# Kernel optimization log

Hardware: AMD Instinct MI355X
Metric: run time of the kernel (lower is better)

## Reference

```python
import jax, jax.numpy as jnp
import numpy as np

B = 256       # number of grasp centers (batch)
N = 65536     # total points output by the backbone
C = 1024      # backbone feature channels (enc_channels[-1])
K = 512       # padded slots per segment (points per center)
INFO = 3      # info_size
KCLS = 6      # k_cls
EPS = 1e-5    # LayerNorm eps


def _layernorm(x, g, b):
    m = x.mean(-1, keepdims=True)
    v = ((x - m) ** 2).mean(-1, keepdims=True)
    return (x - m) / jnp.sqrt(v + EPS) * g + b


def setup_inputs() -> dict:
    key = jax.random.key(0)
    ks = jax.random.split(key, 10)
    feat = jax.random.normal(ks[0], (N, C), jnp.float32)
    offsets = jnp.sort(jax.random.randint(ks[1], (B,), 0, N)).astype(jnp.int64)
    offsets = offsets.at[-1].set(N)  # cumulative ends, last covers all points
    info = jax.random.normal(ks[2], (B, INFO), jnp.float32)

    def lin(k, o, i):
        return 0.02 * jax.random.normal(k, (o, i), jnp.float32), jnp.zeros((o,), jnp.float32)

    W1, b1 = lin(ks[3], 512, C)          # point_layer Linear(1024,512)
    Wi, bi = lin(ks[4], 32, INFO)        # info_layer Linear(info_size,32)
    Wa1, ba1 = lin(ks[5], 256, 544)      # anchor_mlp Linear(544,256)
    Wa2, ba2 = lin(ks[6], KCLS, 256)     # anchor_mlp Linear(256,k_cls)
    Wo1, bo1 = lin(ks[7], 256, 544)      # offset_mlp Linear(544,256)
    Wo2, bo2 = lin(ks[8], KCLS * 3, 256) # offset_mlp Linear(256,k_cls*3)
    return dict(
        feat=feat, info=info, offsets=offsets,
        W1=W1, b1=b1, ln1_g=jnp.ones((512,)), ln1_b=jnp.zeros((512,)),
        Wi=Wi, bi=bi,
        Wa1=Wa1, ba1=ba1, lna_g=jnp.ones((256,)), lna_b=jnp.zeros((256,)),
        Wa2=Wa2, ba2=ba2,
        Wo1=Wo1, bo1=bo1, lno_g=jnp.ones((256,)), lno_b=jnp.zeros((256,)),
        Wo2=Wo2, bo2=bo2,
    )


def reference(feat, info, W1, b1, ln1_g, ln1_b, Wi, bi,
              Wa1, ba1, lna_g, lna_b, Wa2, ba2,
              Wo1, bo1, lno_g, lno_b, Wo2, bo2, offsets):
    # --- fused segment-max replaces the pad loop + max over padded dim ---
    # point i belongs to segment b s.t. offsets[b-1] <= i < offsets[b]
    ids = jnp.searchsorted(offsets, jnp.arange(feat.shape[0]), side='right')
    segmax = jax.ops.segment_max(feat, ids, num_segments=B)  # (B, C)
    lengths = jnp.diff(offsets, prepend=0)
    # original zero-pads to K slots: segments shorter than K see 0 in the max
    features = jnp.where((lengths < K)[:, None], jnp.maximum(segmax, 0.0), segmax)

    # point_layer: Linear -> LayerNorm -> Dropout(eval: identity) -> ReLU
    pf = jax.nn.relu(_layernorm(features @ W1.T + b1, ln1_g, ln1_b))
    # info_layer
    inf = info @ Wi.T + bi
    x = jnp.concatenate([pf, inf], axis=1)  # (B, 544)

    pred = jax.nn.relu(_layernorm(x @ Wa1.T + ba1, lna_g, lna_b)) @ Wa2.T + ba2
    off = jax.nn.relu(_layernorm(x @ Wo1.T + bo1, lno_g, lno_b)) @ Wo2.T + bo2
    offset = off.reshape(-1, KCLS, 3)
    return features, pred, offset
```

## Files before the change

### kernel.cpp

```cpp
#include <hip/hip_runtime.h>
#include <hip/hip_bf16.h>
#include <cstdint>

#define NPTS 65536
#define CCH  1024
#define BSEG 256
#define KSLOT 512

__device__ __forceinline__ int fkey(float f) {
  int i = __float_as_int(f);
  return i >= 0 ? i : (i ^ 0x7FFFFFFF);
}
__device__ __forceinline__ float fdec(int k) {
  int i = k >= 0 ? k : (k ^ 0x7FFFFFFF);
  return __int_as_float(i);
}
#define NEGKEY ((int)0x807FFFFF)

__device__ __forceinline__ float4 max4(float4 a, float4 b) {
  return make_float4(fmaxf(a.x, b.x), fmaxf(a.y, b.y), fmaxf(a.z, b.z), fmaxf(a.w, b.w));
}

__global__ __launch_bounds__(256) void init_keys_k(int* __restrict__ keys) {
  keys[blockIdx.x * 256 + threadIdx.x] = NEGKEY;
}

__global__ __launch_bounds__(256) void segmax_k(const float* __restrict__ feat,
                                                const int* __restrict__ offsets,
                                                int* __restrict__ keys) {
  int t = threadIdx.x;
  int col = t << 2;
  int row0 = blockIdx.x * 64;
  int row_end = row0 + 64;
  int lo = 0, hi = BSEG - 1;
  while (lo < hi) { int mid = (lo + hi) >> 1; if (offsets[mid] > row0) hi = mid; else lo = mid + 1; }
  int seg = lo;
  int end = offsets[seg];
  const float NI = __int_as_float(0xFF800000);
  float4 m = make_float4(NI, NI, NI, NI);
  bool dirty = false;
  int r = row0;
  while (r < row_end) {
    while (r >= end) {
      if (dirty) {
        int* kp = keys + seg * CCH + col;
        atomicMax(kp + 0, fkey(m.x));
        atomicMax(kp + 1, fkey(m.y));
        atomicMax(kp + 2, fkey(m.z));
        atomicMax(kp + 3, fkey(m.w));
        m = make_float4(NI, NI, NI, NI);
        dirty = false;
      }
      ++seg;
      end = offsets[seg];
    }
    int stop = min(row_end, end);
    const float* p = feat + (size_t)r * CCH + col;
    for (; r + 4 <= stop; r += 4) {
      float4 v0 = *(const float4*)(p);
      float4 v1 = *(const float4*)(p + CCH);
      float4 v2 = *(const float4*)(p + 2 * CCH);
      float4 v3 = *(const float4*)(p + 3 * CCH);
      p += 4 * CCH;
      m = max4(m, max4(max4(v0, v1), max4(v2, v3)));
    }
    for (; r < stop; ++r) {
      float4 v = *(const float4*)(p);
      p += CCH;
      m = max4(m, v);
    }
    dirty = true;
  }
  if (dirty) {
    int* kp = keys + seg * CCH + col;
    atomicMax(kp + 0, fkey(m.x));
    atomicMax(kp + 1, fkey(m.y));
    atomicMax(kp + 2, fkey(m.z));
    atomicMax(kp + 3, fkey(m.w));
  }
}

__global__ __launch_bounds__(256) void finalize_k(const int* __restrict__ keys,
                                                  const int* __restrict__ offsets,
                                                  float* __restrict__ outf) {
  int idx = blockIdx.x * 256 + threadIdx.x;
  int b = idx >> 10;
  int len = offsets[b] - (b ? offsets[b - 1] : 0);
  float f = fdec(keys[idx]);
  if (len < KSLOT) f = fmaxf(f, 0.0f);
  outf[idx] = f;
}

__global__ __launch_bounds__(256) void gemm_nt_part(
    const float* __restrict__ A, int lda,
    const float* __restrict__ Wlo, const float* __restrict__ Whi, int nlo, int ldw,
    float* __restrict__ part, int Ktot, int steps_per_chunk) {
  __shared__ float As[32][68];
  __shared__ float Ws[32][68];
  int bx = blockIdx.x, by = blockIdx.y, bz = blockIdx.z;
  int t = threadIdx.x;
  int tx = t & 15, ty = t >> 4;
  int steps_total = Ktot >> 5;
  int step0 = bz * steps_per_chunk;
  int nsteps = min(steps_per_chunk, steps_total - step0);
  int lr = t >> 3;
  int lk = (t & 7) << 2;
  const float* Arow0 = A + (size_t)(by * 64 + lr) * lda + lk;
  const float* Arow1 = Arow0 + (size_t)32 * lda;
  int c0 = bx * 64 + lr;
  int c1 = c0 + 32;
  const float* Wrow0 = (c0 < nlo ? Wlo + (size_t)c0 * ldw : Whi + (size_t)(c0 - nlo) * ldw) + lk;
  const float* Wrow1 = (c1 < nlo ? Wlo + (size_t)c1 * ldw : Whi + (size_t)(c1 - nlo) * ldw) + lk;
  float acc[4][4] = {};
  for (int s = 0; s < nsteps; ++s) {
    int k0 = (step0 + s) << 5;
    float4 a0 = *(const float4*)(Arow0 + k0);
    float4 a1 = *(const float4*)(Arow1 + k0);
    float4 w0 = *(const float4*)(Wrow0 + k0);
    float4 w1 = *(const float4*)(Wrow1 + k0);
    __syncthreads();
    As[lk + 0][lr] = a0.x; As[lk + 1][lr] = a0.y; As[lk + 2][lr] = a0.z; As[lk + 3][lr] = a0.w;
    As[lk + 0][lr + 32] = a1.x; As[lk + 1][lr + 32] = a1.y; As[lk + 2][lr + 32] = a1.z; As[lk + 3][lr + 32] = a1.w;
    Ws[lk + 0][lr] = w0.x; Ws[lk + 1][lr] = w0.y; Ws[lk + 2][lr] = w0.z; Ws[lk + 3][lr] = w0.w;
    Ws[lk + 0][lr + 32] = w1.x; Ws[lk + 1][lr + 32] = w1.y; Ws[lk + 2][lr + 32] = w1.z; Ws[lk + 3][lr + 32] = w1.w;
    __syncthreads();
#pragma unroll
    for (int kk = 0; kk < 32; ++kk) {
      float4 av = *(const float4*)&As[kk][ty << 2];
      float4 wv = *(const float4*)&Ws[kk][tx << 2];
      acc[0][0] += av.x * wv.x; acc[0][1] += av.x * wv.y; acc[0][2] += av.x * wv.z; acc[0][3] += av.x * wv.w;
      acc[1][0] += av.y * wv.x; acc[1][1] += av.y * wv.y; acc[1][2] += av.y * wv.z; acc[1][3] += av.y * wv.w;
      acc[2][0] += av.z * wv.x; acc[2][1] += av.z * wv.y; acc[2][2] += av.z * wv.z; acc[2][3] += av.z * wv.w;
      acc[3][0] += av.w * wv.x; acc[3][1] += av.w * wv.y; acc[3][2] += av.w * wv.z; acc[3][3] += av.w * wv.w;
    }
  }
  float* op = part + (size_t)bz * 131072 + (size_t)(by * 64 + (ty << 2)) * 512 + bx * 64 + (tx << 2);
#pragma unroll
  for (int i = 0; i < 4; ++i) {
    *(float4*)(op + (size_t)i * 512) = make_float4(acc[i][0], acc[i][1], acc[i][2], acc[i][3]);
  }
}

__global__ __launch_bounds__(256) void ln1_x_k(
    const float* __restrict__ part1, const float* __restrict__ b1,
    const float* __restrict__ g, const float* __restrict__ be,
    const float* __restrict__ info, const float* __restrict__ Wi, const float* __restrict__ bi,
    float* __restrict__ x) {
  int b = blockIdx.x, t = threadIdx.x;
  int wv = t >> 6, ln = t & 63;
  __shared__ float red[2][4];
  __shared__ float stats[2];
  const float* p = part1 + (size_t)b * 512;
  float z0 = b1[t] + p[t] + p[131072 + t] + p[262144 + t] + p[393216 + t];
  int c1 = t + 256;
  float z1 = b1[c1] + p[c1] + p[131072 + c1] + p[262144 + c1] + p[393216 + c1];
  float s = z0 + z1, q = z0 * z0 + z1 * z1;
#pragma unroll
  for (int o = 32; o; o >>= 1) { s += __shfl_down(s, o); q += __shfl_down(q, o); }
  if (ln == 0) { red[0][wv] = s; red[1][wv] = q; }
  __syncthreads();
  if (t == 0) {
    float S = red[0][0] + red[0][1] + red[0][2] + red[0][3];
    float Q = red[1][0] + red[1][1] + red[1][2] + red[1][3];
    float mean = S * (1.f / 512.f);
    float var = Q * (1.f / 512.f) - mean * mean;
    stats[0] = mean; stats[1] = rsqrtf(var + 1e-5f);
  }
  __syncthreads();
  float mean = stats[0], rstd = stats[1];
  x[b * 544 + t]  = fmaxf((z0 - mean) * rstd * g[t]  + be[t],  0.f);
  x[b * 544 + c1] = fmaxf((z1 - mean) * rstd * g[c1] + be[c1], 0.f);
  if (t < 32) {
    float i0 = info[b * 3], i1 = info[b * 3 + 1], i2 = info[b * 3 + 2];
    x[b * 544 + 512 + t] = bi[t] + Wi[t * 3] * i0 + Wi[t * 3 + 1] * i1 + Wi[t * 3 + 2] * i2;
  }
}

__global__ __launch_bounds__(256) void heads_k(
    const float* __restrict__ part2,
    const float* __restrict__ ba1, const float* __restrict__ ga, const float* __restrict__ bea,
    const float* __restrict__ Wa2, const float* __restrict__ ba2,
    const float* __restrict__ bo1, const float* __restrict__ go, const float* __restrict__ beo,
    const float* __restrict__ Wo2, const float* __restrict__ bo2,
    float* __restrict__ outp) {
  int b = blockIdx.x, t = threadIdx.x;
  int wv = t >> 6, ln = t & 63;
  __shared__ float h[512];
  __shared__ float red[4][4];
  __shared__ float stats[4];
  const float* p0 = part2 + (size_t)b * 512;
  const float* p1 = p0 + 131072;
  float za = ba1[t] + p0[t] + p1[t];
  float zo = bo1[t] + p0[256 + t] + p1[256 + t];
  float sa = za, qa = za * za, so = zo, qo = zo * zo;
#pragma unroll
  for (int o = 32; o; o >>= 1) {
    sa += __shfl_down(sa, o); qa += __shfl_down(qa, o);
    so += __shfl_down(so, o); qo += __shfl_down(qo, o);
  }
  if (ln == 0) { red[wv][0] = sa; red[wv][1] = qa; red[wv][2] = so; red[wv][3] = qo; }
  __syncthreads();
  if (t == 0) {
    float Sa = red[0][0] + red[1][0] + red[2][0] + red[3][0];
    float Qa = red[0][1] + red[1][1] + red[2][1] + red[3][1];
    float So = red[0][2] + red[1][2] + red[2][2] + red[3][2];
    float Qo = red[0][3] + red[1][3] + red[2][3] + red[3][3];
    float ma = Sa * (1.f / 256.f), va = Qa * (1.f / 256.f) - ma * ma;
    float mo = So * (1.f / 256.f), vo = Qo * (1.f / 256.f) - mo * mo;
    stats[0] = ma; stats[1] = rsqrtf(va + 1e-5f);
    stats[2] = mo; stats[3] = rsqrtf(vo + 1e-5f);
  }
  __syncthreads();
  h[t]       = fmaxf((za - stats[0]) * stats[1] * ga[t] + bea[t], 0.f);
  h[256 + t] = fmaxf((zo - stats[2]) * stats[3] * go[t] + beo[t], 0.f);
  __syncthreads();
  const float* hh = (wv == 0) ? h : (h + 256);
  const float* W2 = (wv == 0) ? Wa2 : Wo2;
  const float* b2 = (wv == 0) ? ba2 : bo2;
  int o0 = (wv == 0) ? 0 : (wv - 1) * 6;
  int base = (wv == 0) ? (262144 + b * 6) : (263680 + b * 18);
  float h0 = hh[ln], h1 = hh[64 + ln], h2v = hh[128 + ln], h3 = hh[192 + ln];
#pragma unroll
  for (int oo = 0; oo < 6; ++oo) {
    int o = o0 + oo;
    const float* w = W2 + o * 256;
    float pr = h0 * w[ln] + h1 * w[64 + ln] + h2v * w[128 + ln] + h3 * w[192 + ln];
#pragma unroll
    for (int d = 32; d; d >>= 1) pr += __shfl_down(pr, d);
    if (ln == 0) outp[base + o] = pr + b2[o];
  }
}

extern "C" void kernel_launch(void* const* d_in, const int* in_sizes, int n_in,
                              void* d_out, int out_size, void* d_ws, size_t ws_size,
                              hipStream_t stream) {
  const float* feat   = (const float*)d_in[0];
  const float* info   = (const float*)d_in[1];
  const int*   offs   = (const int*)d_in[2];
  const float* W1     = (const float*)d_in[3];
  const float* b1     = (const float*)d_in[4];
  const float* ln1_g  = (const float*)d_in[5];
  const float* ln1_b  = (const float*)d_in[6];
  const float* Wi     = (const float*)d_in[7];
  const float* bi     = (const float*)d_in[8];
  const float* Wa1    = (const float*)d_in[9];
  const float* ba1    = (const float*)d_in[10];
  const float* lna_g  = (const float*)d_in[11];
  const float* lna_b  = (const float*)d_in[12];
  const float* Wa2    = (const float*)d_in[13];
  const float* ba2    = (const float*)d_in[14];
  const float* Wo1    = (const float*)d_in[15];
  const float* bo1    = (const float*)d_in[16];
  const float* lno_g  = (const float*)d_in[17];
  const float* lno_b  = (const float*)d_in[18];
  const float* Wo2    = (const float*)d_in[19];
  const float* bo2    = (const float*)d_in[20];

  char* ws = (char*)d_ws;
  int*   keys  = (int*)ws;
  float* part1 = (float*)(ws + (1u << 20));
  float* xbuf  = (float*)(ws + 3u * (1u << 20));
  float* part2 = (float*)(ws + 3u * (1u << 20) + 655360u);
  float* features = (float*)d_out;
  float* outp = (float*)d_out;

  init_keys_k<<<dim3(1024), dim3(256), 0, stream>>>(keys);
  segmax_k<<<dim3(1024), dim3(256), 0, stream>>>(feat, offs, keys);
  finalize_k<<<dim3(1024), dim3(256), 0, stream>>>(keys, offs, features);
  gemm_nt_part<<<dim3(8, 4, 4), dim3(256), 0, stream>>>(
      features, 1024, W1, W1, 512, 1024, part1, 1024, 8);
  ln1_x_k<<<dim3(256), dim3(256), 0, stream>>>(part1, b1, ln1_g, ln1_b, info, Wi, bi, xbuf);
  gemm_nt_part<<<dim3(8, 4, 2), dim3(256), 0, stream>>>(
      xbuf, 544, Wa1, Wo1, 256, 544, part2, 544, 9);
  heads_k<<<dim3(256), dim3(256), 0, stream>>>(
      part2, ba1, lna_g, lna_b, Wa2, ba2, bo1, lno_g, lno_b, Wo2, bo2, outp);
}
```

Before: 99.91 us.

## Fuse segmax finalize into first GEMM, use memset and nontemporal loads

Removes the finalize kernel by decoding the unsigned order-preserving max keys and applying the zero-pad clamp inside the first GEMM's A-tile load. Blocks with bx==0 also write the features output. The key encoding changes to unsigned so a plain hipMemsetAsync of zero can replace the init kernel. The segment-max kernel now covers 32 rows per block with twice as many blocks, unrolls its loop 8 rows deep, and reads feat with nontemporal loads. This cuts two launches and one pass over the key buffer, at the cost of more atomics and redundant decode work in every GEMM block.

```diff
diff --git a/kernel.cpp b/kernel.cpp
--- a/kernel.cpp
+++ b/kernel.cpp
@@ -6,49 +6,57 @@
 #define CCH  1024
 #define BSEG 256
 #define KSLOT 512
-
-__device__ __forceinline__ int fkey(float f) {
+#define WROWS 32
+
+typedef float v4f __attribute__((ext_vector_type(4)));
+
+__device__ __forceinline__ unsigned ukey(float f) {
   int i = __float_as_int(f);
-  return i >= 0 ? i : (i ^ 0x7FFFFFFF);
-}
-__device__ __forceinline__ float fdec(int k) {
-  int i = k >= 0 ? k : (k ^ 0x7FFFFFFF);
-  return __int_as_float(i);
-}
-#define NEGKEY ((int)0x807FFFFF)
-
-__device__ __forceinline__ float4 max4(float4 a, float4 b) {
-  return make_float4(fmaxf(a.x, b.x), fmaxf(a.y, b.y), fmaxf(a.z, b.z), fmaxf(a.w, b.w));
-}
-
-__global__ __launch_bounds__(256) void init_keys_k(int* __restrict__ keys) {
-  keys[blockIdx.x * 256 + threadIdx.x] = NEGKEY;
+  return i >= 0 ? ((unsigned)i | 0x80000000u) : ~(unsigned)i;
+}
+__device__ __forceinline__ float udec(unsigned u, bool rl) {
+  float v;
+  if (u >= 0x80000000u) v = __int_as_float((int)(u & 0x7FFFFFFFu));
+  else                  v = __int_as_float((int)~u);
+  if (u == 0u) v = -__builtin_inff();
+  if (rl) v = fmaxf(v, 0.0f);
+  return v;
+}
+
+__device__ __forceinline__ v4f ntload4(const float* p) {
+  return __builtin_nontemporal_load((const v4f*)p);
+}
+__device__ __forceinline__ v4f vmax4(v4f a, v4f b) {
+  v4f r;
+  r.x = fmaxf(a.x, b.x); r.y = fmaxf(a.y, b.y);
+  r.z = fmaxf(a.z, b.z); r.w = fmaxf(a.w, b.w);
+  return r;
 }
 
 __global__ __launch_bounds__(256) void segmax_k(const float* __restrict__ feat,
                                                 const int* __restrict__ offsets,
-                                                int* __restrict__ keys) {
+                                                unsigned* __restrict__ keys) {
   int t = threadIdx.x;
   int col = t << 2;
-  int row0 = blockIdx.x * 64;
-  int row_end = row0 + 64;
+  int row0 = blockIdx.x * WROWS;
+  int row_end = row0 + WROWS;
   int lo = 0, hi = BSEG - 1;
   while (lo < hi) { int mid = (lo + hi) >> 1; if (offsets[mid] > row0) hi = mid; else lo = mid + 1; }
   int seg = lo;
   int end = offsets[seg];
-  const float NI = __int_as_float(0xFF800000);
-  float4 m = make_float4(NI, NI, NI, NI);
+  const float NI = -__builtin_inff();
+  v4f m; m.x = NI; m.y = NI; m.z = NI; m.w = NI;
   bool dirty = false;
   int r = row0;
   while (r < row_end) {
     while (r >= end) {
       if (dirty) {
-        int* kp = keys + seg * CCH + col;
-        atomicMax(kp + 0, fkey(m.x));
-        atomicMax(kp + 1, fkey(m.y));
-        atomicMax(kp + 2, fkey(m.z));
-        atomicMax(kp + 3, fkey(m.w));
-        m = make_float4(NI, NI, NI, NI);
+        unsigned* kp = keys + (size_t)seg * CCH + col;
+        atomicMax(kp + 0, ukey(m.x));
+        atomicMax(kp + 1, ukey(m.y));
+        atomicMax(kp + 2, ukey(m.z));
+        atomicMax(kp + 3, ukey(m.w));
+        m.x = NI; m.y = NI; m.z = NI; m.w = NI;
         dirty = false;
       }
       ++seg;
@@ -56,39 +64,89 @@
     }
     int stop = min(row_end, end);
     const float* p = feat + (size_t)r * CCH + col;
-    for (; r + 4 <= stop; r += 4) {
-      float4 v0 = *(const float4*)(p);
-      float4 v1 = *(const float4*)(p + CCH);
-      float4 v2 = *(const float4*)(p + 2 * CCH);
-      float4 v3 = *(const float4*)(p + 3 * CCH);
-      p += 4 * CCH;
-      m = max4(m, max4(max4(v0, v1), max4(v2, v3)));
+    for (; r + 8 <= stop; r += 8) {
+      v4f v0 = ntload4(p);
+      v4f v1 = ntload4(p + CCH);
+      v4f v2 = ntload4(p + 2 * CCH);
+      v4f v3 = ntload4(p + 3 * CCH);
+      v4f v4 = ntload4(p + 4 * CCH);
+      v4f v5 = ntload4(p + 5 * CCH);
+      v4f v6 = ntload4(p + 6 * CCH);
+      v4f v7 = ntload4(p + 7 * CCH);
+      p += 8 * CCH;
+      m = vmax4(m, vmax4(vmax4(vmax4(v0, v1), vmax4(v2, v3)),
+                         vmax4(vmax4(v4, v5), vmax4(v6, v7))));
     }
     for (; r < stop; ++r) {
-      float4 v = *(const float4*)(p);
+      v4f v = ntload4(p);
       p += CCH;
-      m = max4(m, v);
+      m = vmax4(m, v);
     }
     dirty = true;
   }
   if (dirty) {
-    int* kp = keys + seg * CCH + col;
-    atomicMax(kp + 0, fkey(m.x));
-    atomicMax(kp + 1, fkey(m.y));
-    atomicMax(kp + 2, fkey(m.z));
-    atomicMax(kp + 3, fkey(m.w));
-  }
-}
-
-__global__ __launch_bounds__(256) void finalize_k(const int* __restrict__ keys,
-                                                  const int* __restrict__ offsets,
-                                                  float* __restrict__ outf) {
-  int idx = blockIdx.x * 256 + threadIdx.x;
-  int b = idx >> 10;
-  int len = offsets[b] - (b ? offsets[b - 1] : 0);
-  float f = fdec(keys[idx]);
-  if (len < KSLOT) f = fmaxf(f, 0.0f);
-  outf[idx] = f;
+    unsigned* kp = keys + (size_t)seg * CCH + col;
+    atomicMax(kp + 0, ukey(m.x));
+    atomicMax(kp + 1, ukey(m.y));
+    atomicMax(kp + 2, ukey(m.z));
+    atomicMax(kp + 3, ukey(m.w));
+  }
+}
+
+__global__ __launch_bounds__(256) void gemm1_fused(
+    const unsigned* __restrict__ keys, const int* __restrict__ offsets,
+    const float* __restrict__ W1, float* __restrict__ features,
+    float* __restrict__ part) {
+  __shared__ float As[32][68];
+  __shared__ float Ws[32][68];
+  int bx = blockIdx.x, by = blockIdx.y, bz = blockIdx.z;
+  int t = threadIdx.x;
+  int tx = t & 15, ty = t >> 4;
+  int lr = t >> 3;
+  int lk = (t & 7) << 2;
+  int row0 = by * 64 + lr, row1 = row0 + 32;
+  int len0 = offsets[row0] - (row0 ? offsets[row0 - 1] : 0);
+  int len1 = offsets[row1] - offsets[row1 - 1];
+  bool rl0 = len0 < KSLOT, rl1 = len1 < KSLOT;
+  const unsigned* K0 = keys + (size_t)row0 * CCH + lk;
+  const unsigned* K1 = keys + (size_t)row1 * CCH + lk;
+  int c0 = bx * 64 + lr, c1 = c0 + 32;
+  const float* Wr0 = W1 + (size_t)c0 * CCH + lk;
+  const float* Wr1 = W1 + (size_t)c1 * CCH + lk;
+  float acc[4][4] = {};
+  for (int s = 0; s < 8; ++s) {
+    int k0 = (bz * 8 + s) << 5;
+    uint4 ua = *(const uint4*)(K0 + k0);
+    uint4 ub = *(const uint4*)(K1 + k0);
+    float4 w0 = *(const float4*)(Wr0 + k0);
+    float4 w1 = *(const float4*)(Wr1 + k0);
+    float4 a0 = make_float4(udec(ua.x, rl0), udec(ua.y, rl0), udec(ua.z, rl0), udec(ua.w, rl0));
+    float4 a1 = make_float4(udec(ub.x, rl1), udec(ub.y, rl1), udec(ub.z, rl1), udec(ub.w, rl1));
+    if (bx == 0) {
+      *(float4*)(features + (size_t)row0 * CCH + k0 + lk) = a0;
+      *(float4*)(features + (size_t)row1 * CCH + k0 + lk) = a1;
+    }
+    __syncthreads();
+    As[lk + 0][lr] = a0.x; As[lk + 1][lr] = a0.y; As[lk + 2][lr] = a0.z; As[lk + 3][lr] = a0.w;
+    As[lk + 0][lr + 32] = a1.x; As[lk + 1][lr + 32] = a1.y; As[lk + 2][lr + 32] = a1.z; As[lk + 3][lr + 32] = a1.w;
+    Ws[lk + 0][lr] = w0.x; Ws[lk + 1][lr] = w0.y; Ws[lk + 2][lr] = w0.z; Ws[lk + 3][lr] = w0.w;
+    Ws[lk + 0][lr + 32] = w1.x; Ws[lk + 1][lr + 32] = w1.y; Ws[lk + 2][lr + 32] = w1.z; Ws[lk + 3][lr + 32] = w1.w;
+    __syncthreads();
+#pragma unroll
+    for (int kk = 0; kk < 32; ++kk) {
+      float4 av = *(const float4*)&As[kk][ty << 2];
+      float4 wv = *(const float4*)&Ws[kk][tx << 2];
+      acc[0][0] += av.x * wv.x; acc[0][1] += av.x * wv.y; acc[0][2] += av.x * wv.z; acc[0][3] += av.x * wv.w;
+      acc[1][0] += av.y * wv.x; acc[1][1] += av.y * wv.y; acc[1][2] += av.y * wv.z; acc[1][3] += av.y * wv.w;
+      acc[2][0] += av.z * wv.x; acc[2][1] += av.z * wv.y; acc[2][2] += av.z * wv.z; acc[2][3] += av.z * wv.w;
+      acc[3][0] += av.w * wv.x; acc[3][1] += av.w * wv.y; acc[3][2] += av.w * wv.z; acc[3][3] += av.w * wv.w;
+    }
+  }
+  float* op = part + (size_t)bz * 131072 + (size_t)(by * 64 + (ty << 2)) * 512 + bx * 64 + (tx << 2);
+#pragma unroll
+  for (int i = 0; i < 4; ++i) {
+    *(float4*)(op + (size_t)i * 512) = make_float4(acc[i][0], acc[i][1], acc[i][2], acc[i][3]);
+  }
 }
 
 __global__ __launch_bounds__(256) void gemm_nt_part(
@@ -257,18 +315,16 @@
   const float* bo2    = (const float*)d_in[20];
 
   char* ws = (char*)d_ws;
-  int*   keys  = (int*)ws;
+  unsigned* keys  = (unsigned*)ws;
   float* part1 = (float*)(ws + (1u << 20));
   float* xbuf  = (float*)(ws + 3u * (1u << 20));
   float* part2 = (float*)(ws + 3u * (1u << 20) + 655360u);
   float* features = (float*)d_out;
   float* outp = (float*)d_out;
 
-  init_keys_k<<<dim3(1024), dim3(256), 0, stream>>>(keys);
-  segmax_k<<<dim3(1024), dim3(256), 0, stream>>>(feat, offs, keys);
-  finalize_k<<<dim3(1024), dim3(256), 0, stream>>>(keys, offs, features);
-  gemm_nt_part<<<dim3(8, 4, 4), dim3(256), 0, stream>>>(
-      features, 1024, W1, W1, 512, 1024, part1, 1024, 8);
+  hipMemsetAsync(keys, 0, (size_t)BSEG * CCH * sizeof(unsigned), stream);
+  segmax_k<<<dim3(NPTS / WROWS), dim3(256), 0, stream>>>(feat, offs, keys);
+  gemm1_fused<<<dim3(8, 4, 4), dim3(256), 0, stream>>>(keys, offs, W1, features, part1);
   ln1_x_k<<<dim3(256), dim3(256), 0, stream>>>(part1, b1, ln1_g, ln1_b, info, Wi, bi, xbuf);
   gemm_nt_part<<<dim3(8, 4, 2), dim3(256), 0, stream>>>(
       xbuf, 544, Wa1, Wo1, 256, 544, part2, 544, 9);
```

Measured after the change: 104.5 us. +4.6%, slower.
